# Kernel optimization log

Measured on AMD Instinct MI355X. Metric: run time of the kernel, lower is better.

## Reference

```python
import jax, jax.numpy as jnp
import numpy as np

N, E, D_IN, D_H, D_OUT = 100000, 1600000, 128, 128, 47
BN_EPS = 1e-5


def setup_inputs() -> dict:
    key = jax.random.key(0)
    ks = jax.random.split(key, 12)
    x = jax.random.normal(ks[0], (N, D_IN), dtype=jnp.float32)
    edge_index = jax.random.randint(ks[1], (2, E), 0, N, dtype=jnp.int64)
    s = 1.0 / np.sqrt(D_H)
    return {
        "x": x,
        "edge_index": edge_index,
        "W1": jax.random.normal(ks[2], (D_IN, D_H), dtype=jnp.float32) * s,
        "b1": jnp.zeros((D_H,), dtype=jnp.float32),
        "gamma": jax.random.uniform(ks[3], (D_H,), dtype=jnp.float32, minval=0.5, maxval=1.5),
        "beta": jax.random.normal(ks[4], (D_H,), dtype=jnp.float32) * 0.1,
        "mean": jax.random.normal(ks[5], (D_H,), dtype=jnp.float32) * 0.1,
        "var": jax.random.uniform(ks[6], (D_H,), dtype=jnp.float32, minval=0.5, maxval=1.5),
        "W2": jax.random.normal(ks[7], (D_H, D_H), dtype=jnp.float32) * s,
        "b2": jnp.zeros((D_H,), dtype=jnp.float32),
        "Wf": jax.random.normal(ks[8], (D_H, D_OUT), dtype=jnp.float32) * s,
        "bf": jnp.zeros((D_OUT,), dtype=jnp.float32),
    }


def gcn_conv(x, src, dst, W, b, n):
    # x' = x @ W, then symmetric-normalized aggregation with self-loops (PyG GCNConv).
    h = x @ W
    loops = jnp.arange(n, dtype=src.dtype)
    s = jnp.concatenate([src, loops])
    d = jnp.concatenate([dst, loops])
    deg = jax.ops.segment_sum(jnp.ones_like(d, dtype=h.dtype), d, num_segments=n)
    dinv = jnp.where(deg > 0, jax.lax.rsqrt(deg), 0.0)
    norm = dinv[s] * dinv[d]                      # [E+N]
    msg = h[s] * norm[:, None]                    # [E+N, D] gather
    out = jax.ops.segment_sum(msg, d, num_segments=n)  # scatter-add
    return out + b


def reference(x, edge_index, W1, b1, gamma, beta, mean, var, W2, b2, Wf, bf):
    n = x.shape[0]
    src, dst = edge_index[0], edge_index[1]
    # layer 1: GCNConv -> BatchNorm (eval) -> ReLU -> dropout (identity in eval)
    h1 = gcn_conv(x, src, dst, W1, b1, n)
    h1 = (h1 - mean) * jax.lax.rsqrt(var + BN_EPS) * gamma + beta
    h1 = jax.nn.relu(h1)
    # layer 2 (last conv, no BN/act)
    h2 = gcn_conv(h1, src, dst, W2, b2, n)
    # JumpingKnowledge max over layer outputs
    jk = jnp.maximum(h1, h2)
    logits = jk @ Wf + bf
    return jax.nn.log_softmax(logits, axis=1)
```

## Files before the change

kernel.cpp:

```cpp
#include <hip/hip_runtime.h>
#include <math.h>

#define DH 128
#define DOUT 47
#define BN_EPS 1e-5f

typedef __attribute__((ext_vector_type(8))) short short8;
typedef __attribute__((ext_vector_type(4))) float float4v;
typedef __attribute__((ext_vector_type(2))) float float2v;

__device__ __forceinline__ unsigned bf16_rne(float f) {
    unsigned u = __float_as_uint(f);
    return (u + 0x7fffu + ((u >> 16) & 1u)) >> 16;
}
__device__ __forceinline__ unsigned pack_bf2(float a, float b) {
    return (bf16_rne(a) & 0xffffu) | (bf16_rne(b) << 16);
}
__device__ __forceinline__ float2 unpack_bf2(unsigned u) {
    return make_float2(__uint_as_float(u << 16),
                       __uint_as_float(u & 0xffff0000u));
}


__global__ __launch_bounds__(256) void prep_k(const float* __restrict__ W1,
                                              const float* __restrict__ W2,
                                              unsigned* __restrict__ W1b,
                                              unsigned* __restrict__ W2b,
                                              int* __restrict__ countsP,
                                              unsigned* __restrict__ bufA, int n) {
    int tid = threadIdx.x;
    if (blockIdx.x >= 2) {
        int i4 = (blockIdx.x - 2) * 256 + tid;
        if (i4 < n * 4) *(int4*)(countsP + (size_t)i4 * 4) = make_int4(0, 0, 0, 0);
        return;
    }
    const float* W = blockIdx.x ? W2 : W1;
    unsigned* Wb = blockIdx.x ? W2b : W1b;
    if (blockIdx.x == 0 && tid < 64) bufA[(size_t)n * 64 + tid] = 0;
    for (int p = tid; p < 128 * 32; p += 256) {
        int nn = p >> 5;
        int k0 = (p & 31) << 2;
        float f0 = W[(size_t)(k0 + 0) * 128 + nn];
        float f1 = W[(size_t)(k0 + 1) * 128 + nn];
        float f2 = W[(size_t)(k0 + 2) * 128 + nn];
        float f3 = W[(size_t)(k0 + 3) * 128 + nn];
        uint2 v;
        v.x = pack_bf2(f0, f1);
        v.y = pack_bf2(f2, f3);
        *(uint2*)(Wb + (size_t)nn * 64 + (k0 >> 1)) = v;
    }
}

__global__ __launch_bounds__(256) void fused_gc_k(
    const float* __restrict__ A, const unsigned* __restrict__ Wb,
    unsigned* __restrict__ Cb, int M,
    const int* __restrict__ dst, int* __restrict__ countsP,
    int* __restrict__ rank, int e, int gemmBlocks) {
    __shared__ ushort Bl[128 * 136];
    int bid = blockIdx.x;
    int r3 = bid % 3;
    int q3 = bid / 3;
    int tid = threadIdx.x;

    if (r3 == 2) {
        int i0 = (q3 * 256 + tid) * 8;
        if (i0 + 8 <= e) {
            int4 d4 = *(const int4*)(dst + i0);
            int4 e4 = *(const int4*)(dst + i0 + 4);
            int4 r4, s4;
            r4.x = atomicAdd(&countsP[(size_t)d4.x * 16], 1);
            r4.y = atomicAdd(&countsP[(size_t)d4.y * 16], 1);
            r4.z = atomicAdd(&countsP[(size_t)d4.z * 16], 1);
            r4.w = atomicAdd(&countsP[(size_t)d4.w * 16], 1);
            s4.x = atomicAdd(&countsP[(size_t)e4.x * 16], 1);
            s4.y = atomicAdd(&countsP[(size_t)e4.y * 16], 1);
            s4.z = atomicAdd(&countsP[(size_t)e4.z * 16], 1);
            s4.w = atomicAdd(&countsP[(size_t)e4.w * 16], 1);
            *(int4*)(rank + i0) = r4;
            *(int4*)(rank + i0 + 4) = s4;
        } else {
            for (int i = i0; i < e; i++)
                rank[i] = atomicAdd(&countsP[(size_t)dst[i] * 16], 1);
        }
        return;
    }

    int gIdx = q3 * 2 + r3;
    if (gIdx >= gemmBlocks) return;
    {
        unsigned* Bu = (unsigned*)Bl;
        for (int q = tid; q < 128 * 16; q += 256) {
            int row = q >> 4;
            int c = (q & 15) << 2;
            uint4 v = *(const uint4*)(Wb + (size_t)row * 64 + c);
            *(uint4*)(Bu + (size_t)row * 68 + c) = v;
        }
    }
    __syncthreads();

    int lane = tid & 63;
    int wv = tid >> 6;
    int quad = lane >> 4;
    int l15 = lane & 15;
    int r0 = gIdx * 64 + wv * 16;
    int mload = r0 + l15;
    if (mload > M - 1) mload = M - 1;
    const float* Ar = A + (size_t)mload * 128 + quad * 8;

    float4v acc[8];
#pragma unroll
    for (int t = 0; t < 8; t++) acc[t] = (float4v){0.f, 0.f, 0.f, 0.f};

    for (int kp = 0; kp < 4; ++kp) {
        float4 a0 = *(const float4*)(Ar + kp * 32);
        float4 a1 = *(const float4*)(Ar + kp * 32 + 4);
        float af[8] = {a0.x, a0.y, a0.z, a0.w, a1.x, a1.y, a1.z, a1.w};
        short8 av;
#pragma unroll
        for (int j = 0; j < 8; j++) av[j] = (short)bf16_rne(af[j]);
        int kb = kp * 32 + quad * 8;
#pragma unroll
        for (int nt = 0; nt < 8; nt++) {
            short8 b8 = *(const short8*)(&Bl[(size_t)(nt * 16 + l15) * 136 + kb]);
            acc[nt] = __builtin_amdgcn_mfma_f32_16x16x32_bf16(av, b8, acc[nt], 0, 0, 0);
        }
    }

    ushort* Cu = (ushort*)Cb;
#pragma unroll
    for (int r = 0; r < 4; r++) {
        int row = r0 + quad * 4 + r;
        if (row < M) {
#pragma unroll
            for (int nt = 0; nt < 8; nt++) {
                Cu[(size_t)row * 128 + nt * 16 + l15] =
                    (ushort)bf16_rne(acc[nt][r]);
            }
        }
    }
}

__global__ __launch_bounds__(256) void scan1_k(const int* __restrict__ countsP,
                                               int* __restrict__ offsets,
                                               int* __restrict__ blocksums, int n) {
    __shared__ int sd[256];
    int tid = threadIdx.x;
    int base = blockIdx.x * 1024 + tid * 4;
    int v0 = (base + 0 < n) ? ((countsP[(size_t)(base + 0) * 16] + 7) & ~7) : 0;
    int v1 = (base + 1 < n) ? ((countsP[(size_t)(base + 1) * 16] + 7) & ~7) : 0;
    int v2 = (base + 2 < n) ? ((countsP[(size_t)(base + 2) * 16] + 7) & ~7) : 0;
    int v3 = (base + 3 < n) ? ((countsP[(size_t)(base + 3) * 16] + 7) & ~7) : 0;
    int tsum = v0 + v1 + v2 + v3;
    sd[tid] = tsum;
    __syncthreads();
    for (int off = 1; off < 256; off <<= 1) {
        int x = (tid >= off) ? sd[tid - off] : 0;
        __syncthreads();
        sd[tid] += x;
        __syncthreads();
    }
    if (tid == 255) blocksums[blockIdx.x] = sd[255];
    int run = sd[tid] - tsum;
    if (base + 0 < n) offsets[base + 0] = run;  run += v0;
    if (base + 1 < n) offsets[base + 1] = run;  run += v1;
    if (base + 2 < n) offsets[base + 2] = run;  run += v2;
    if (base + 3 < n) offsets[base + 3] = run;
}

__global__ __launch_bounds__(128) void scan2_k(int* __restrict__ blocksums, int nb,
                                               int* __restrict__ el, int n) {
    __shared__ int sd[128];
    int tid = threadIdx.x;
    int v = (tid < nb) ? blocksums[tid] : 0;
    sd[tid] = v;
    __syncthreads();
    for (int off = 1; off < 128; off <<= 1) {
        int x = (tid >= off) ? sd[tid - off] : 0;
        __syncthreads();
        sd[tid] += x;
        __syncthreads();
    }
    if (tid < nb) blocksums[tid] = sd[tid] - v;
    int total = sd[127];
    if (tid < 96) el[total + tid] = n;
}

__global__ void finalize_k(int* __restrict__ offsets,
                           float* __restrict__ dinv, const int* __restrict__ countsP,
                           const int* __restrict__ blocksums,
                           int* __restrict__ el, int n) {
    int i = blockIdx.x * 256 + threadIdx.x;
    if (i >= n) return;
    int o = offsets[i] + blocksums[i >> 10];
    offsets[i] = o;
    int c = countsP[(size_t)i * 16];
    dinv[i] = rsqrtf((float)(c + 1));
    int cP = (c + 7) & ~7;
    for (int j = o + c; j < o + cP; ++j) el[j] = n;
}

__global__ __launch_bounds__(256) void scatter_k(const int* __restrict__ src,
                                                 const int* __restrict__ dst,
                                                 const int* __restrict__ rank,
                                                 const int* __restrict__ offsets,
                                                 const float* __restrict__ dinv,
                                                 int* __restrict__ el, int e) {
    int i0 = (blockIdx.x * 256 + threadIdx.x) * 4;
    if (i0 + 4 <= e) {
        int4 s4 = *(const int4*)(src + i0);
        int4 d4 = *(const int4*)(dst + i0);
        int4 r4 = *(const int4*)(rank + i0);
        unsigned qx = (unsigned)(dinv[s4.x] * 32767.f + 0.5f);
        unsigned qy = (unsigned)(dinv[s4.y] * 32767.f + 0.5f);
        unsigned qz = (unsigned)(dinv[s4.z] * 32767.f + 0.5f);
        unsigned qw = (unsigned)(dinv[s4.w] * 32767.f + 0.5f);
        el[offsets[d4.x] + r4.x] = (int)((unsigned)s4.x | (qx << 17));
        el[offsets[d4.y] + r4.y] = (int)((unsigned)s4.y | (qy << 17));
        el[offsets[d4.z] + r4.z] = (int)((unsigned)s4.z | (qz << 17));
        el[offsets[d4.w] + r4.w] = (int)((unsigned)s4.w | (qw << 17));
    } else {
        for (int i = i0; i < e; i++) {
            unsigned q = (unsigned)(dinv[src[i]] * 32767.f + 0.5f);
            el[offsets[dst[i]] + rank[i]] = (int)((unsigned)src[i] | (q << 17));
        }
    }
}

__global__ __launch_bounds__(256) void gemm_bf16_k(const unsigned* __restrict__ Ab,
                                                   const unsigned* __restrict__ Wb,
                                                   unsigned* __restrict__ Cb, int M) {
    __shared__ ushort Bl[128 * 136];
    int tid = threadIdx.x;
    {
        unsigned* Bu = (unsigned*)Bl;
        for (int q = tid; q < 128 * 16; q += 256) {
            int row = q >> 4;
            int c = (q & 15) << 2;
            uint4 v = *(const uint4*)(Wb + (size_t)row * 64 + c);
            *(uint4*)(Bu + (size_t)row * 68 + c) = v;
        }
    }
    __syncthreads();

    int lane = tid & 63;
    int wv = tid >> 6;
    int quad = lane >> 4;
    int l15 = lane & 15;
    int r0 = blockIdx.x * 64 + wv * 16;
    int mload = r0 + l15;
    if (mload > M - 1) mload = M - 1;
    const unsigned* Ar = Ab + (size_t)mload * 64 + quad * 4;

    float4v acc[8];
#pragma unroll
    for (int t = 0; t < 8; t++) acc[t] = (float4v){0.f, 0.f, 0.f, 0.f};

    for (int kp = 0; kp < 4; ++kp) {
        uint4 a4 = *(const uint4*)(Ar + kp * 16);
        short8 av;
        av[0] = (short)(a4.x & 0xffff); av[1] = (short)(a4.x >> 16);
        av[2] = (short)(a4.y & 0xffff); av[3] = (short)(a4.y >> 16);
        av[4] = (short)(a4.z & 0xffff); av[5] = (short)(a4.z >> 16);
        av[6] = (short)(a4.w & 0xffff); av[7] = (short)(a4.w >> 16);
        int kb = kp * 32 + quad * 8;
#pragma unroll
        for (int nt = 0; nt < 8; nt++) {
            short8 b8 = *(const short8*)(&Bl[(size_t)(nt * 16 + l15) * 136 + kb]);
            acc[nt] = __builtin_amdgcn_mfma_f32_16x16x32_bf16(av, b8, acc[nt], 0, 0, 0);
        }
    }

    ushort* Cu = (ushort*)Cb;
#pragma unroll
    for (int r = 0; r < 4; r++) {
        int row = r0 + quad * 4 + r;
        if (row < M) {
#pragma unroll
            for (int nt = 0; nt < 8; nt++) {
                Cu[(size_t)row * 128 + nt * 16 + l15] =
                    (ushort)bf16_rne(acc[nt][r]);
            }
        }
    }
}

__device__ __forceinline__ float4 agg_core(const uint2* __restrict__ Hu2,
                                           const int* __restrict__ el,
                                           int start, int cnt, int node,
                                           float dvn, int li, int half) {
    float2v a01 = {0.f, 0.f};
    float2v a23 = {0.f, 0.f};
    int groups = ((cnt + 7) & ~7) >> 3;
    if (groups > 0) {
        const int* p = el + start + half * 4;

#define EDGE(cu, rr) {                                                       \
        float qf = (float)((unsigned)(rr) >> 17) * (1.f / 32767.f);          \
        float2v f0, f1;                                                      \
        f0.x = __uint_as_float((cu).x << 16);                                \
        f0.y = __uint_as_float((cu).x & 0xffff0000u);                        \
        f1.x = __uint_as_float((cu).y << 16);                                \
        f1.y = __uint_as_float((cu).y & 0xffff0000u);                        \
        a01.x = fmaf(f0.x, qf, a01.x); a01.y = fmaf(f0.y, qf, a01.y);        \
        a23.x = fmaf(f1.x, qf, a23.x); a23.y = fmaf(f1.y, qf, a23.y);        \
}
        int4 rc = *(const int4*)p;
        uint2 c0 = Hu2[(size_t)(rc.x & 0x1FFFF) * 32 + li];
        uint2 c1 = Hu2[(size_t)(rc.y & 0x1FFFF) * 32 + li];
        uint2 c2 = Hu2[(size_t)(rc.z & 0x1FFFF) * 32 + li];
        uint2 c3 = Hu2[(size_t)(rc.w & 0x1FFFF) * 32 + li];
        int4 rn = *(const int4*)(p + 8);
        for (int g = 0; g < groups; ++g) {
            uint2 n0 = Hu2[(size_t)(rn.x & 0x1FFFF) * 32 + li];
            uint2 n1 = Hu2[(size_t)(rn.y & 0x1FFFF) * 32 + li];
            uint2 n2 = Hu2[(size_t)(rn.z & 0x1FFFF) * 32 + li];
            uint2 n3 = Hu2[(size_t)(rn.w & 0x1FFFF) * 32 + li];
            int4 r2 = *(const int4*)(p + 8 * (g + 2));
            EDGE(c0, rc.x) EDGE(c1, rc.y) EDGE(c2, rc.z) EDGE(c3, rc.w)
            c0 = n0; c1 = n1; c2 = n2; c3 = n3;
            rc = rn; rn = r2;
        }
#undef EDGE
    }
    float4 acc = make_float4(a01.x, a01.y, a23.x, a23.y);
    acc.x += __shfl_xor(acc.x, 32);
    acc.y += __shfl_xor(acc.y, 32);
    acc.z += __shfl_xor(acc.z, 32);
    acc.w += __shfl_xor(acc.w, 32);
    uint2 sv = Hu2[(size_t)node * 32 + li];
    float2 s0 = unpack_bf2(sv.x);
    float2 s1 = unpack_bf2(sv.y);
    acc.x = fmaf(s0.x, dvn, acc.x); acc.y = fmaf(s0.y, dvn, acc.y);
    acc.z = fmaf(s1.x, dvn, acc.z); acc.w = fmaf(s1.y, dvn, acc.w);
    return acc;
}

__global__ __launch_bounds__(256) void agg1_k(
    const unsigned* __restrict__ H, const int* __restrict__ el,
    const int* __restrict__ offsets, const int* __restrict__ counts,
    const float* __restrict__ dinv, const float* __restrict__ b1,
    const float* __restrict__ gamma, const float* __restrict__ beta,
    const float* __restrict__ mean, const float* __restrict__ var,
    unsigned* __restrict__ H1b, int n) {
    int lane = threadIdx.x & 63;
    int li = lane & 31;
    int half = lane >> 5;
    int node = blockIdx.x * 4 + (threadIdx.x >> 6);
    if (node >= n) return;
    float dv = dinv[node];
    float4 acc = agg_core((const uint2*)H, el, offsets[node],
                          counts[(size_t)node * 16], node, dv, li, half);
    if (half == 0) {
        int f0 = li * 4;
        float4 bb = *(const float4*)(b1 + f0);
        float4 mm = *(const float4*)(mean + f0);
        float4 vv = *(const float4*)(var + f0);
        float4 gg = *(const float4*)(gamma + f0);
        float4 be = *(const float4*)(beta + f0);
        float4 o;
        o.x = fmaxf((acc.x * dv + bb.x - mm.x) * rsqrtf(vv.x + BN_EPS) * gg.x + be.x, 0.f);
        o.y = fmaxf((acc.y * dv + bb.y - mm.y) * rsqrtf(vv.y + BN_EPS) * gg.y + be.y, 0.f);
        o.z = fmaxf((acc.z * dv + bb.z - mm.z) * rsqrtf(vv.z + BN_EPS) * gg.z + be.z, 0.f);
        o.w = fmaxf((acc.w * dv + bb.w - mm.w) * rsqrtf(vv.w + BN_EPS) * gg.w + be.w, 0.f);
        uint2 pk;
        pk.x = pack_bf2(o.x, o.y);
        pk.y = pack_bf2(o.z, o.w);
        *(uint2*)(H1b + (size_t)node * 64 + li * 2) = pk;
    }
}

__global__ __launch_bounds__(256) void agg2_k(
    const unsigned* __restrict__ H, const int* __restrict__ el,
    const int* __restrict__ offsets, const int* __restrict__ counts,
    const float* __restrict__ dinv, const float* __restrict__ b2,
    unsigned* __restrict__ H1b, int n) {
    int lane = threadIdx.x & 63;
    int li = lane & 31;
    int half = lane >> 5;
    int node = blockIdx.x * 4 + (threadIdx.x >> 6);
    if (node >= n) return;
    float dv = dinv[node];
    float4 acc = agg_core((const uint2*)H, el, offsets[node],
                          counts[(size_t)node * 16], node, dv, li, half);
    if (half == 0) {
        int f0 = li * 4;
        float4 bb = *(const float4*)(b2 + f0);
        uint2* p = (uint2*)(H1b + (size_t)node * 64 + li * 2);
        uint2 hv = *p;
        float2 ha = unpack_bf2(hv.x);
        float2 hb = unpack_bf2(hv.y);
        float4 o;
        o.x = fmaxf(ha.x, acc.x * dv + bb.x);
        o.y = fmaxf(ha.y, acc.y * dv + bb.y);
        o.z = fmaxf(hb.x, acc.z * dv + bb.z);
        o.w = fmaxf(hb.y, acc.w * dv + bb.w);
        uint2 pk;
        pk.x = pack_bf2(o.x, o.y);
        pk.y = pack_bf2(o.z, o.w);
        *p = pk;
    }
}

__global__ __launch_bounds__(256) void head_k(const unsigned* __restrict__ JKb,
                                              const float* __restrict__ Wf,
                                              const float* __restrict__ bf,
                                              float* __restrict__ out, int n) {
    __shared__ __align__(16) float Bs[48 * 132];
    __shared__ __align__(16) float As[64 * 36];
    int tid = threadIdx.x;
    for (int p = tid; p < 47 * 32; p += 256) {
        int c = p >> 5;
        int k0 = (p & 31) << 2;
        float4 v;
        v.x = Wf[(size_t)(k0 + 0) * DOUT + c];
        v.y = Wf[(size_t)(k0 + 1) * DOUT + c];
        v.z = Wf[(size_t)(k0 + 2) * DOUT + c];
        v.w = Wf[(size_t)(k0 + 3) * DOUT + c];
        *(float4*)(&Bs[c * 132 + k0]) = v;
    }
    int tx = tid & 15;
    int ty = tid >> 4;
    int node0 = blockIdx.x * 64;

    float acc[4][3];
#pragma unroll
    for (int i = 0; i < 4; i++)
#pragma unroll
        for (int j = 0; j < 3; j++) acc[i][j] = 0.f;

    for (int kk = 0; kk < 128; kk += 32) {
        __syncthreads();
        for (int l = tid; l < 512; l += 256) {
            int r = l >> 3;
            int c4 = (l & 7) << 2;
            int row = node0 + r;
            float4 v = make_float4(0.f, 0.f, 0.f, 0.f);
            if (row < n) {
                uint2 u = *(const uint2*)(JKb + (size_t)row * 64 + ((kk + c4) >> 1));
                float2 f0 = unpack_bf2(u.x);
                float2 f1 = unpack_bf2(u.y);
                v = make_float4(f0.x, f0.y, f1.x, f1.y);
            }
            *(float4*)(&As[r * 36 + c4]) = v;
        }
        __syncthreads();
#pragma unroll
        for (int k4 = 0; k4 < 32; k4 += 4) {
            float4 a0 = *(const float4*)(&As[(ty * 4 + 0) * 36 + k4]);
            float4 a1 = *(const float4*)(&As[(ty * 4 + 1) * 36 + k4]);
            float4 a2 = *(const float4*)(&As[(ty * 4 + 2) * 36 + k4]);
            float4 a3 = *(const float4*)(&As[(ty * 4 + 3) * 36 + k4]);
            float4 b0 = *(const float4*)(&Bs[(tx * 3 + 0) * 132 + kk + k4]);
            float4 b1 = *(const float4*)(&Bs[(tx * 3 + 1) * 132 + kk + k4]);
            float4 b2 = *(const float4*)(&Bs[(tx * 3 + 2) * 132 + kk + k4]);
#define DOT_ROW(i, a)                                                        \
            acc[i][0] = fmaf(a.x, b0.x, acc[i][0]);                          \
            acc[i][0] = fmaf(a.y, b0.y, acc[i][0]);                          \
            acc[i][0] = fmaf(a.z, b0.z, acc[i][0]);                          \
            acc[i][0] = fmaf(a.w, b0.w, acc[i][0]);                          \
            acc[i][1] = fmaf(a.x, b1.x, acc[i][1]);                          \
            acc[i][1] = fmaf(a.y, b1.y, acc[i][1]);                          \
            acc[i][1] = fmaf(a.z, b1.z, acc[i][1]);                          \
            acc[i][1] = fmaf(a.w, b1.w, acc[i][1]);                          \
            acc[i][2] = fmaf(a.x, b2.x, acc[i][2]);                          \
            acc[i][2] = fmaf(a.y, b2.y, acc[i][2]);                          \
            acc[i][2] = fmaf(a.z, b2.z, acc[i][2]);                          \
            acc[i][2] = fmaf(a.w, b2.w, acc[i][2]);
            DOT_ROW(0, a0)
            DOT_ROW(1, a1)
            DOT_ROW(2, a2)
            DOT_ROW(3, a3)
#undef DOT_ROW
        }
    }

    float bfv[3];
#pragma unroll
    for (int j = 0; j < 3; j++) {
        int c = tx * 3 + j;
        bfv[j] = (c < DOUT) ? bf[c] : 0.f;
    }
#pragma unroll
    for (int i = 0; i < 4; i++) {
        int node = node0 + ty * 4 + i;
        float l0 = acc[i][0] + bfv[0];
        float l1 = acc[i][1] + bfv[1];
        float l2 = acc[i][2] + bfv[2];
        bool v2ok = (tx * 3 + 2) < DOUT;
        float m = fmaxf(l0, l1);
        if (v2ok) m = fmaxf(m, l2);
        for (int off = 8; off >= 1; off >>= 1) m = fmaxf(m, __shfl_xor(m, off));
        float s = expf(l0 - m) + expf(l1 - m) + (v2ok ? expf(l2 - m) : 0.f);
        for (int off = 8; off >= 1; off >>= 1) s += __shfl_xor(s, off);
        float ls = m + logf(s);
        if (node < n) {
            float* o = out + (size_t)node * DOUT + tx * 3;
            o[0] = l0 - ls;
            o[1] = l1 - ls;
            if (v2ok) o[2] = l2 - ls;
        }
    }
}

extern "C" void kernel_launch(void* const* d_in, const int* in_sizes, int n_in,
                              void* d_out, int out_size, void* d_ws, size_t ws_size,
                              hipStream_t stream) {
    const float* x     = (const float*)d_in[0];
    const int*   ei    = (const int*)d_in[1];
    const float* W1    = (const float*)d_in[2];
    const float* b1    = (const float*)d_in[3];
    const float* gamma = (const float*)d_in[4];
    const float* beta  = (const float*)d_in[5];
    const float* mean  = (const float*)d_in[6];
    const float* var   = (const float*)d_in[7];
    const float* W2    = (const float*)d_in[8];
    const float* b2    = (const float*)d_in[9];
    const float* Wf    = (const float*)d_in[10];
    const float* bf    = (const float*)d_in[11];
    float* out = (float*)d_out;

    int N_ = in_sizes[0] / 128;
    int E_ = in_sizes[1] / 2;
    const int* src = ei;
    const int* dst = ei + E_;

    char* ws = (char*)d_ws;
    unsigned* bufA = (unsigned*)ws; ws += (size_t)(N_ + 1) * 64 * 4;
    unsigned* h1b  = (unsigned*)ws; ws += (size_t)N_ * 64 * 4;
    int* countsP   = (int*)ws;    ws += (size_t)N_ * 16 * 4;
    int*   offsets = (int*)ws;    ws += (size_t)N_ * 4;
    float* dinv    = (float*)ws;  ws += (size_t)N_ * 4;
    int*   rank    = (int*)ws;    ws += (size_t)E_ * 4;
    int*   el      = (int*)ws;    ws += ((size_t)E_ + 7 * (size_t)N_ + 128) * 4;
    int*   bsums   = (int*)ws;    ws += 1024 * 4;
    unsigned* W1b  = (unsigned*)ws; ws += 128 * 64 * 4;
    unsigned* W2b  = (unsigned*)ws; ws += 128 * 64 * 4;

    int nb = (N_ + 1023) / 1024;
    int gemmBlocks = (N_ + 63) / 64;
    int countBlocks = (E_ + 2047) / 2048;
    int pairs = countBlocks > (gemmBlocks + 1) / 2 ? countBlocks : (gemmBlocks + 1) / 2;
    int fusedGrid = 3 * pairs;
    int edgeBlocks = (E_ + 1023) / 1024;
    int zeroBlocks = (N_ * 4 + 255) / 256;

    prep_k<<<2 + zeroBlocks, 256, 0, stream>>>(W1, W2, W1b, W2b, countsP, bufA, N_);
    fused_gc_k<<<fusedGrid, 256, 0, stream>>>(x, W1b, bufA, N_,
                                              dst, countsP, rank, E_, gemmBlocks);
    scan1_k<<<nb, 256, 0, stream>>>(countsP, offsets, bsums, N_);
    scan2_k<<<1, 128, 0, stream>>>(bsums, nb, el, N_);
    finalize_k<<<(N_ + 255) / 256, 256, 0, stream>>>(offsets, dinv,
                                                     countsP, bsums, el, N_);
    scatter_k<<<edgeBlocks, 256, 0, stream>>>(src, dst, rank, offsets, dinv, el, E_);

    agg1_k<<<(N_ + 3) / 4, 256, 0, stream>>>(bufA, el, offsets, countsP, dinv,
                                             b1, gamma, beta, mean, var, h1b, N_);
    gemm_bf16_k<<<gemmBlocks, 256, 0, stream>>>(h1b, W2b, bufA, N_);
    agg2_k<<<(N_ + 3) / 4, 256, 0, stream>>>(bufA, el, offsets, countsP, dinv,
                                             b2, h1b, N_);
    head_k<<<(N_ + 63) / 64, 256, 0, stream>>>(h1b, Wf, bf, out, N_);
}
```

Measured before the change: 414.2 us.

## Privatize degree-count atomics per XCC with workgroup-scope atomics and tagged ranks

```diff
diff --git a/kernel.cpp b/kernel.cpp
--- a/kernel.cpp
+++ b/kernel.cpp
@@ -26,12 +26,12 @@
                                               const float* __restrict__ W2,
                                               unsigned* __restrict__ W1b,
                                               unsigned* __restrict__ W2b,
-                                              int* __restrict__ countsP,
+                                              int* __restrict__ counts8,
                                               unsigned* __restrict__ bufA, int n) {
     int tid = threadIdx.x;
     if (blockIdx.x >= 2) {
         int i4 = (blockIdx.x - 2) * 256 + tid;
-        if (i4 < n * 4) *(int4*)(countsP + (size_t)i4 * 4) = make_int4(0, 0, 0, 0);
+        if (i4 < n * 2) *(int4*)(counts8 + (size_t)i4 * 4) = make_int4(0, 0, 0, 0);
         return;
     }
     const float* W = blockIdx.x ? W2 : W1;
@@ -51,11 +51,17 @@
     }
 }
 
+__device__ __forceinline__ int xcc_id() {
+    int x;
+    asm volatile("s_getreg_b32 %0, hwreg(HW_REG_XCC_ID)" : "=s"(x));
+    return x & 7;
+}
+
 __global__ __launch_bounds__(256) void fused_gc_k(
     const float* __restrict__ A, const unsigned* __restrict__ Wb,
     unsigned* __restrict__ Cb, int M,
-    const int* __restrict__ dst, int* __restrict__ countsP,
-    int* __restrict__ rank, int e, int gemmBlocks) {
+    const int* __restrict__ dst, int* __restrict__ counts8,
+    int* __restrict__ rank, int e, int gemmBlocks, int n) {
     __shared__ ushort Bl[128 * 136];
     int bid = blockIdx.x;
     int r3 = bid % 3;
@@ -63,25 +69,30 @@
     int tid = threadIdx.x;
 
     if (r3 == 2) {
+        int xcc = xcc_id();
+        int* cnt = counts8 + (size_t)xcc * n;
+        int tag = xcc << 24;
         int i0 = (q3 * 256 + tid) * 8;
+#define CADD(d) ((int)__hip_atomic_fetch_add(&cnt[(d)], 1, __ATOMIC_RELAXED, \
+                                             __HIP_MEMORY_SCOPE_WORKGROUP) | tag)
         if (i0 + 8 <= e) {
             int4 d4 = *(const int4*)(dst + i0);
             int4 e4 = *(const int4*)(dst + i0 + 4);
             int4 r4, s4;
-            r4.x = atomicAdd(&countsP[(size_t)d4.x * 16], 1);
-            r4.y = atomicAdd(&countsP[(size_t)d4.y * 16], 1);
-            r4.z = atomicAdd(&countsP[(size_t)d4.z * 16], 1);
-            r4.w = atomicAdd(&countsP[(size_t)d4.w * 16], 1);
-            s4.x = atomicAdd(&countsP[(size_t)e4.x * 16], 1);
-            s4.y = atomicAdd(&countsP[(size_t)e4.y * 16], 1);
-            s4.z = atomicAdd(&countsP[(size_t)e4.z * 16], 1);
-            s4.w = atomicAdd(&countsP[(size_t)e4.w * 16], 1);
+            r4.x = CADD(d4.x);
+            r4.y = CADD(d4.y);
+            r4.z = CADD(d4.z);
+            r4.w = CADD(d4.w);
+            s4.x = CADD(e4.x);
+            s4.y = CADD(e4.y);
+            s4.z = CADD(e4.z);
+            s4.w = CADD(e4.w);
             *(int4*)(rank + i0) = r4;
             *(int4*)(rank + i0 + 4) = s4;
         } else {
-            for (int i = i0; i < e; i++)
-                rank[i] = atomicAdd(&countsP[(size_t)dst[i] * 16], 1);
-        }
+            for (int i = i0; i < e; i++) rank[i] = CADD(dst[i]);
+        }
+#undef CADD
         return;
     }
 
@@ -140,17 +151,25 @@
     }
 }
 
-__global__ __launch_bounds__(256) void scan1_k(const int* __restrict__ countsP,
+__global__ __launch_bounds__(256) void scan1_k(const int* __restrict__ counts8,
                                                int* __restrict__ offsets,
                                                int* __restrict__ blocksums, int n) {
     __shared__ int sd[256];
     int tid = threadIdx.x;
     int base = blockIdx.x * 1024 + tid * 4;
-    int v0 = (base + 0 < n) ? ((countsP[(size_t)(base + 0) * 16] + 7) & ~7) : 0;
-    int v1 = (base + 1 < n) ? ((countsP[(size_t)(base + 1) * 16] + 7) & ~7) : 0;
-    int v2 = (base + 2 < n) ? ((countsP[(size_t)(base + 2) * 16] + 7) & ~7) : 0;
-    int v3 = (base + 3 < n) ? ((countsP[(size_t)(base + 3) * 16] + 7) & ~7) : 0;
-    int tsum = v0 + v1 + v2 + v3;
+    int v[4];
+#pragma unroll
+    for (int j = 0; j < 4; j++) {
+        int idx = base + j;
+        int c = 0;
+        if (idx < n) {
+#pragma unroll
+            for (int r = 0; r < 8; r++) c += counts8[(size_t)r * n + idx];
+            c = (c + 7) & ~7;
+        }
+        v[j] = c;
+    }
+    int tsum = v[0] + v[1] + v[2] + v[3];
     sd[tid] = tsum;
     __syncthreads();
     for (int off = 1; off < 256; off <<= 1) {
@@ -161,9 +180,9 @@
     }
     if (tid == 255) blocksums[blockIdx.x] = sd[255];
     int run = sd[tid] - tsum;
-    if (base + 0 < n) offsets[base + 0] = run;  run += v0;
-    if (base + 1 < n) offsets[base + 1] = run;  run += v1;
-    if (base + 2 < n) offsets[base + 2] = run;  run += v2;
+    if (base + 0 < n) offsets[base + 0] = run;  run += v[0];
+    if (base + 1 < n) offsets[base + 1] = run;  run += v[1];
+    if (base + 2 < n) offsets[base + 2] = run;  run += v[2];
     if (base + 3 < n) offsets[base + 3] = run;
 }
 
@@ -186,14 +205,22 @@
 }
 
 __global__ void finalize_k(int* __restrict__ offsets,
-                           float* __restrict__ dinv, const int* __restrict__ countsP,
+                           float* __restrict__ dinv, int* __restrict__ counts8,
                            const int* __restrict__ blocksums,
+                           int* __restrict__ base8,
                            int* __restrict__ el, int n) {
     int i = blockIdx.x * 256 + threadIdx.x;
     if (i >= n) return;
     int o = offsets[i] + blocksums[i >> 10];
     offsets[i] = o;
-    int c = countsP[(size_t)i * 16];
+    int run = o;
+#pragma unroll
+    for (int r = 0; r < 8; r++) {
+        base8[(size_t)i * 8 + r] = run;
+        run += counts8[(size_t)r * n + i];
+    }
+    int c = run - o;
+    counts8[i] = c;
     dinv[i] = rsqrtf((float)(c + 1));
     int cP = (c + 7) & ~7;
     for (int j = o + c; j < o + cP; ++j) el[j] = n;
@@ -202,7 +229,7 @@
 __global__ __launch_bounds__(256) void scatter_k(const int* __restrict__ src,
                                                  const int* __restrict__ dst,
                                                  const int* __restrict__ rank,
-                                                 const int* __restrict__ offsets,
+                                                 const int* __restrict__ base8,
                                                  const float* __restrict__ dinv,
                                                  int* __restrict__ el, int e) {
     int i0 = (blockIdx.x * 256 + threadIdx.x) * 4;
@@ -214,14 +241,20 @@
         unsigned qy = (unsigned)(dinv[s4.y] * 32767.f + 0.5f);
         unsigned qz = (unsigned)(dinv[s4.z] * 32767.f + 0.5f);
         unsigned qw = (unsigned)(dinv[s4.w] * 32767.f + 0.5f);
-        el[offsets[d4.x] + r4.x] = (int)((unsigned)s4.x | (qx << 17));
-        el[offsets[d4.y] + r4.y] = (int)((unsigned)s4.y | (qy << 17));
-        el[offsets[d4.z] + r4.z] = (int)((unsigned)s4.z | (qz << 17));
-        el[offsets[d4.w] + r4.w] = (int)((unsigned)s4.w | (qw << 17));
+        int ix = base8[(size_t)d4.x * 8 + (((unsigned)r4.x >> 24) & 7)] + (r4.x & 0xFFFFFF);
+        int iy = base8[(size_t)d4.y * 8 + (((unsigned)r4.y >> 24) & 7)] + (r4.y & 0xFFFFFF);
+        int iz = base8[(size_t)d4.z * 8 + (((unsigned)r4.z >> 24) & 7)] + (r4.z & 0xFFFFFF);
+        int iw = base8[(size_t)d4.w * 8 + (((unsigned)r4.w >> 24) & 7)] + (r4.w & 0xFFFFFF);
+        el[ix] = (int)((unsigned)s4.x | (qx << 17));
+        el[iy] = (int)((unsigned)s4.y | (qy << 17));
+        el[iz] = (int)((unsigned)s4.z | (qz << 17));
+        el[iw] = (int)((unsigned)s4.w | (qw << 17));
     } else {
         for (int i = i0; i < e; i++) {
             unsigned q = (unsigned)(dinv[src[i]] * 32767.f + 0.5f);
-            el[offsets[dst[i]] + rank[i]] = (int)((unsigned)src[i] | (q << 17));
+            int rw = rank[i];
+            int idx = base8[(size_t)dst[i] * 8 + (((unsigned)rw >> 24) & 7)] + (rw & 0xFFFFFF);
+            el[idx] = (int)((unsigned)src[i] | (q << 17));
         }
     }
 }
@@ -349,7 +382,7 @@
     if (node >= n) return;
     float dv = dinv[node];
     float4 acc = agg_core((const uint2*)H, el, offsets[node],
-                          counts[(size_t)node * 16], node, dv, li, half);
+                          counts[node], node, dv, li, half);
     if (half == 0) {
         int f0 = li * 4;
         float4 bb = *(const float4*)(b1 + f0);
@@ -381,7 +414,7 @@
     if (node >= n) return;
     float dv = dinv[node];
     float4 acc = agg_core((const uint2*)H, el, offsets[node],
-                          counts[(size_t)node * 16], node, dv, li, half);
+                          counts[node], node, dv, li, half);
     if (half == 0) {
         int f0 = li * 4;
         float4 bb = *(const float4*)(b2 + f0);
@@ -527,7 +560,8 @@
     char* ws = (char*)d_ws;
     unsigned* bufA = (unsigned*)ws; ws += (size_t)(N_ + 1) * 64 * 4;
     unsigned* h1b  = (unsigned*)ws; ws += (size_t)N_ * 64 * 4;
-    int* countsP   = (int*)ws;    ws += (size_t)N_ * 16 * 4;
+    int* counts8   = (int*)ws;    ws += (size_t)N_ * 8 * 4;
+    int* base8     = (int*)ws;    ws += (size_t)N_ * 8 * 4;
     int*   offsets = (int*)ws;    ws += (size_t)N_ * 4;
     float* dinv    = (float*)ws;  ws += (size_t)N_ * 4;
     int*   rank    = (int*)ws;    ws += (size_t)E_ * 4;
@@ -542,21 +576,21 @@
     int pairs = countBlocks > (gemmBlocks + 1) / 2 ? countBlocks : (gemmBlocks + 1) / 2;
     int fusedGrid = 3 * pairs;
     int edgeBlocks = (E_ + 1023) / 1024;
-    int zeroBlocks = (N_ * 4 + 255) / 256;
-
-    prep_k<<<2 + zeroBlocks, 256, 0, stream>>>(W1, W2, W1b, W2b, countsP, bufA, N_);
+    int zeroBlocks = (N_ * 2 + 255) / 256;
+
+    prep_k<<<2 + zeroBlocks, 256, 0, stream>>>(W1, W2, W1b, W2b, counts8, bufA, N_);
     fused_gc_k<<<fusedGrid, 256, 0, stream>>>(x, W1b, bufA, N_,
-                                              dst, countsP, rank, E_, gemmBlocks);
-    scan1_k<<<nb, 256, 0, stream>>>(countsP, offsets, bsums, N_);
+                                              dst, counts8, rank, E_, gemmBlocks, N_);
+    scan1_k<<<nb, 256, 0, stream>>>(counts8, offsets, bsums, N_);
     scan2_k<<<1, 128, 0, stream>>>(bsums, nb, el, N_);
     finalize_k<<<(N_ + 255) / 256, 256, 0, stream>>>(offsets, dinv,
-                                                     countsP, bsums, el, N_);
-    scatter_k<<<edgeBlocks, 256, 0, stream>>>(src, dst, rank, offsets, dinv, el, E_);
-
-    agg1_k<<<(N_ + 3) / 4, 256, 0, stream>>>(bufA, el, offsets, countsP, dinv,
+                                                     counts8, bsums, base8, el, N_);
+    scatter_k<<<edgeBlocks, 256, 0, stream>>>(src, dst, rank, base8, dinv, el, E_);
+
+    agg1_k<<<(N_ + 3) / 4, 256, 0, stream>>>(bufA, el, offsets, counts8, dinv,
                                              b1, gamma, beta, mean, var, h1b, N_);
     gemm_bf16_k<<<gemmBlocks, 256, 0, stream>>>(h1b, W2b, bufA, N_);
-    agg2_k<<<(N_ + 3) / 4, 256, 0, stream>>>(bufA, el, offsets, countsP, dinv,
+    agg2_k<<<(N_ + 3) / 4, 256, 0, stream>>>(bufA, el, offsets, counts8, dinv,
                                              b2, h1b, N_);
     head_k<<<(N_ + 63) / 64, 256, 0, stream>>>(h1b, Wf, bf, out, N_);
 }
```

New measurement: 420.4 us. About the same (+1.5%).
